# Performance work log

Hardware: AMD Instinct MI355X
Metric: run time of the kernel (lower is better)

## Reference

```python
import jax, jax.numpy as jnp
import numpy as np

B, H, S, D = 2, 16, 2048, 64  # depth = dmodel / num_heads
DMODEL = H * D


def setup_inputs() -> dict:
    key = jax.random.key(0)
    kq, kk, kv, kw = jax.random.split(key, 4)
    Q = jax.random.normal(kq, (B, H, S, D), dtype=jnp.float32)
    K = jax.random.normal(kk, (B, H, S, D), dtype=jnp.float32)
    V = jax.random.normal(kv, (B, H, S, D), dtype=jnp.float32)
    W = jax.random.normal(kw, (DMODEL, DMODEL), dtype=jnp.float32) * (1.0 / np.sqrt(DMODEL))
    b = jnp.zeros((DMODEL,), dtype=jnp.float32)
    return {"Q": Q, "K": K, "V": V, "W": W, "b": b}


def reference(Q, K, V, W, b):
    depth = Q.shape[-1]
    # scores: (B, H, S, S) -- full score matrix, matching the original math
    scores = jnp.einsum('bhqd,bhkd->bhqk', Q, K) / jnp.sqrt(jnp.float32(depth))
    attn = jax.nn.softmax(scores, axis=-1)
    vals = jnp.einsum('bhqk,bhkd->bhqd', attn, V)          # (B, H, S, D)
    vals = jnp.transpose(vals, (0, 2, 1, 3))               # (B, S, H, D)
    concat = vals.reshape(vals.shape[0], vals.shape[1], -1)  # (B, S, dmodel)
    return concat @ W + b
```

## Files before the change

kernel.cpp:

```cpp
#include <hip/hip_runtime.h>
#include <hip/hip_bf16.h>


typedef float  f32x16 __attribute__((ext_vector_type(16)));
typedef float  f32x4v __attribute__((ext_vector_type(4)));
typedef float  f32x2v __attribute__((ext_vector_type(2)));
typedef __bf16 bf16x8 __attribute__((ext_vector_type(8)));
typedef __bf16 bf16x4 __attribute__((ext_vector_type(4)));
typedef __bf16 bf16x2 __attribute__((ext_vector_type(2)));

static constexpr int Bn = 2, Hn = 16, Sn = 2048, Dn = 64, DM = 1024;
static constexpr size_t QKV_ELEMS = (size_t)Bn * Hn * Sn * Dn;

#define QSCALE 0.18033688011112042f

#if __has_builtin(__builtin_amdgcn_cvt_pk_bf16_f32)
static __device__ __forceinline__ unsigned pack2(float a, float b) {
  bf16x2 t = __builtin_amdgcn_cvt_pk_bf16_f32(a, b);
  union { bf16x2 v; unsigned u; } c; c.v = t; return c.u;
}
#else
static __device__ __forceinline__ unsigned pack2(float a, float b) {
  union { __bf16 h; unsigned short s; } ua, ub;
  ua.h = (__bf16)a; ub.h = (__bf16)b;
  return (unsigned)ua.s | ((unsigned)ub.s << 16);
}
#endif

static __device__ __forceinline__ void unzip8(const unsigned* wds, bf16x8* r0, bf16x8* r1) {
  union { unsigned u[4]; bf16x8 v; } a, b;
#pragma unroll
  for (int i = 0; i < 4; ++i) {
    unsigned lo = wds[2 * i], hi = wds[2 * i + 1];
    a.u[i] = (lo & 0xffffu) | (hi << 16);
    b.u[i] = (lo >> 16) | (hi & 0xffff0000u);
  }
  *r0 = a.v; *r1 = b.v;
}

__global__ __launch_bounds__(256) void convert_all(
    const float* __restrict__ q, const float* __restrict__ k,
    const float* __restrict__ v, const float* __restrict__ w,
    __bf16* __restrict__ qo, __bf16* __restrict__ ko,
    __bf16* __restrict__ vt, __bf16* __restrict__ wt) {
  __shared__ __bf16 T[64][74];
  const int bid = blockIdx.x, t = threadIdx.x;

  if (bid < 4096) {
    const int z = bid >> 11;
    const int bx = bid & 2047;
    const float* src = z ? k : q;
    __bf16* dst      = z ? ko : qo;
    const float scale = z ? 1.0f : QSCALE;
    size_t i = ((size_t)bx * 256 + t) * 8;
    f32x4v a = *(const f32x4v*)(src + i);
    f32x4v b = *(const f32x4v*)(src + i + 4);
    bf16x8 o;
#pragma unroll
    for (int j = 0; j < 4; ++j) { o[j] = (__bf16)(a[j] * scale); o[4 + j] = (__bf16)(b[j] * scale); }
    *(bf16x8*)(dst + i) = o;
    return;
  }

  const float* s0;
  __bf16* dst0;
  size_t dst_stride;
  {
    const int r = t >> 2, c0 = (t & 3) * 16;
    if (bid < 5120) {
      const int idx = bid - 4096;
      const int kv0 = (idx & 31) * 64, bh = idx >> 5;
      s0 = v + ((size_t)bh * Sn + kv0 + r) * Dn + c0;
      dst0 = vt + (size_t)bh * Dn * Sn + kv0;
      dst_stride = Sn;
    } else {
      const int idx = bid - 5120;
      const int nt = (idx & 15) * 64, kt = (idx >> 4) * 64;
      s0 = w + (size_t)(kt + r) * DM + nt + c0;
      dst0 = wt + (size_t)nt * DM + kt;
      dst_stride = DM;
    }
    union { bf16x8 v8; unsigned u[4]; } o0, o1;
#pragma unroll
    for (int i = 0; i < 2; ++i) {
      f32x4v f = *(const f32x4v*)(s0 + i * 4);
#pragma unroll
      for (int j = 0; j < 4; ++j) o0.v8[i * 4 + j] = (__bf16)f[j];
    }
#pragma unroll
    for (int i = 0; i < 2; ++i) {
      f32x4v f = *(const f32x4v*)(s0 + 8 + i * 4);
#pragma unroll
      for (int j = 0; j < 4; ++j) o1.v8[i * 4 + j] = (__bf16)f[j];
    }
#pragma unroll
    for (int j = 0; j < 4; ++j) {
      *(unsigned*)&T[r][c0 + 2 * j]     = o0.u[j];
      *(unsigned*)&T[r][c0 + 8 + 2 * j] = o1.u[j];
    }
  }
  __syncthreads();
  const int rp = t >> 3, k0 = (t & 7) * 8;
  unsigned wds[8];
#pragma unroll
  for (int i = 0; i < 8; ++i) wds[i] = *(const unsigned*)&T[k0 + i][2 * rp];
  bf16x8 r0, r1; unzip8(wds, &r0, &r1);
  __bf16* d0 = dst0 + (size_t)(2 * rp) * dst_stride + k0;
  *(bf16x8*)d0 = r0;
  *(bf16x8*)(d0 + dst_stride) = r1;
}

__global__ __launch_bounds__(256, 3) void attn(
    const __bf16* __restrict__ Qb, const __bf16* __restrict__ Kb,
    const __bf16* __restrict__ Vtg, __bf16* __restrict__ Cc) {
  const int tid = threadIdx.x;
  const int wave = tid >> 6, lane = tid & 63;
  const int ln = lane & 31, g = lane >> 5;
  const int qg = wave >> 1, kh = wave & 1;
  const int qb = blockIdx.x, h = blockIdx.y, bz = blockIdx.z;

  __shared__ __bf16 smem[2][2][64][72];
  __bf16 (*Ks)[64][72] = smem[0];
  __bf16 (*Vs)[64][72] = smem[1];

  const size_t hoff = (size_t)(bz * Hn + h) * Sn * Dn;
  const __bf16* Qp = Qb + hoff + (size_t)(qb * 128 + qg * 64) * Dn;
  const __bf16* Kp = Kb + hoff;
  const __bf16* Vp = Vtg + hoff;

  bf16x8 qf[2][4];
#pragma unroll
  for (int qt = 0; qt < 2; ++qt)
#pragma unroll
    for (int ks = 0; ks < 4; ++ks)
      qf[qt][ks] = *(const bf16x8*)(Qp + (size_t)(qt * 32 + ln) * Dn + ks * 16 + g * 8);

  const int sr = tid >> 2, sc = (tid & 3) * 16;
  const __bf16* kbase = Kp + (size_t)sr * Dn + sc;
  const __bf16* vbase = Vp + (size_t)sr * Sn + sc;

  bf16x8 k0r = *(const bf16x8*)kbase, k1r = *(const bf16x8*)(kbase + 8);
  bf16x8 v0r = *(const bf16x8*)vbase, v1r = *(const bf16x8*)(vbase + 8);
  *(bf16x8*)&Ks[0][sr][sc]     = k0r;
  *(bf16x8*)&Ks[0][sr][sc + 8] = k1r;
  *(bf16x8*)&Vs[0][sr][sc]     = v0r;
  *(bf16x8*)&Vs[0][sr][sc + 8] = v1r;
  k0r = *(const bf16x8*)(kbase + (size_t)64 * Dn);
  k1r = *(const bf16x8*)(kbase + (size_t)64 * Dn + 8);
  v0r = *(const bf16x8*)(vbase + 64);
  v1r = *(const bf16x8*)(vbase + 64 + 8);
  __syncthreads();

  f32x16 O[2][2] = {{{}, {}}, {{}, {}}};
  float Lown[2] = {0.0f, 0.0f};
  constexpr int NT = Sn / 64;

  for (int kt = 0; kt < NT; ++kt) {
    const int buf = kt & 1;

    bf16x8 kf[4];
#pragma unroll
    for (int ks = 0; ks < 4; ++ks)
      kf[ks] = *(const bf16x8*)&Ks[buf][kh * 32 + ln][ks * 16 + g * 8];

    unsigned w[2][8];
#pragma unroll
    for (int qt = 0; qt < 2; ++qt) {
      f32x16 s = {};
#pragma unroll
      for (int ks = 0; ks < 4; ++ks)
        s = __builtin_amdgcn_mfma_f32_32x32x16_bf16(kf[ks], qf[qt][ks], s, 0, 0, 0);
      float p[16];
#pragma unroll
      for (int r = 0; r < 16; ++r) p[r] = __builtin_amdgcn_exp2f(s[r]);
      f32x2v s2 = {0.0f, 0.0f};
#pragma unroll
      for (int tt = 0; tt < 8; ++tt) { f32x2v t2 = {p[2 * tt], p[2 * tt + 1]}; s2 += t2; }
      Lown[qt] += s2[0] + s2[1];
#pragma unroll
      for (int tt = 0; tt < 8; ++tt) w[qt][tt] = pack2(p[2 * tt], p[2 * tt + 1]);
    }

    if (kt + 1 < NT) {
      const int nb = buf ^ 1;
      *(bf16x8*)&Ks[nb][sr][sc]     = k0r;
      *(bf16x8*)&Ks[nb][sr][sc + 8] = k1r;
      *(bf16x8*)&Vs[nb][sr][sc]     = v0r;
      *(bf16x8*)&Vs[nb][sr][sc + 8] = v1r;
      if (kt + 2 < NT) {
        const __bf16* kp = kbase + (size_t)(kt + 2) * 64 * Dn;
        k0r = *(const bf16x8*)kp; k1r = *(const bf16x8*)(kp + 8);
        const __bf16* vp = vbase + (kt + 2) * 64;
        v0r = *(const bf16x8*)vp; v1r = *(const bf16x8*)(vp + 8);
      }
    }

#pragma unroll
    for (int s4 = 0; s4 < 2; ++s4) {
      const int cb = kh * 32 + s4 * 16 + g * 4;
      union { bf16x4 h[2]; bf16x8 v; } vf0, vf1;
      vf0.h[0] = *(const bf16x4*)&Vs[buf][ln][cb];
      vf0.h[1] = *(const bf16x4*)&Vs[buf][ln][cb + 8];
      vf1.h[0] = *(const bf16x4*)&Vs[buf][32 + ln][cb];
      vf1.h[1] = *(const bf16x4*)&Vs[buf][32 + ln][cb + 8];
#pragma unroll
      for (int qt = 0; qt < 2; ++qt) {
        union { unsigned u[4]; bf16x8 v; } pu;
        pu.u[0] = w[qt][s4 * 4 + 0];
        pu.u[1] = w[qt][s4 * 4 + 1];
        pu.u[2] = w[qt][s4 * 4 + 2];
        pu.u[3] = w[qt][s4 * 4 + 3];
        O[qt][0] = __builtin_amdgcn_mfma_f32_32x32x16_bf16(vf0.v, pu.v, O[qt][0], 0, 0, 0);
        O[qt][1] = __builtin_amdgcn_mfma_f32_32x32x16_bf16(vf1.v, pu.v, O[qt][1], 0, 0, 0);
      }
    }
    __syncthreads();
  }

  float Lred[2];
#pragma unroll
  for (int qt = 0; qt < 2; ++qt) Lred[qt] = Lown[qt] + __shfl_xor(Lown[qt], 32);

  float* Ex = (float*)smem;
  const int slot = (qg * 64 + lane) * 68;
  if (kh == 1) {
#pragma unroll
    for (int qt = 0; qt < 2; ++qt)
#pragma unroll
      for (int dh = 0; dh < 2; ++dh)
#pragma unroll
        for (int i = 0; i < 4; ++i) {
          f32x4v t = {O[qt][dh][4 * i], O[qt][dh][4 * i + 1],
                      O[qt][dh][4 * i + 2], O[qt][dh][4 * i + 3]};
          *(f32x4v*)&Ex[slot + qt * 32 + dh * 16 + 4 * i] = t;
        }
    Ex[slot + 64] = Lred[0];
    Ex[slot + 65] = Lred[1];
  }
  __syncthreads();
  float inv[2] = {0.0f, 0.0f};
  if (kh == 0) {
#pragma unroll
    for (int qt = 0; qt < 2; ++qt)
#pragma unroll
      for (int dh = 0; dh < 2; ++dh)
#pragma unroll
        for (int i = 0; i < 4; ++i) {
          f32x4v t = *(const f32x4v*)&Ex[slot + qt * 32 + dh * 16 + 4 * i];
#pragma unroll
          for (int c = 0; c < 4; ++c) O[qt][dh][4 * i + c] += t[c];
        }
    inv[0] = 1.0f / (Lred[0] + Ex[slot + 64]);
    inv[1] = 1.0f / (Lred[1] + Ex[slot + 65]);
  }
  __syncthreads();
  __bf16* T = (__bf16*)smem;
  if (kh == 0) {
#pragma unroll
    for (int qt = 0; qt < 2; ++qt)
#pragma unroll
      for (int dh = 0; dh < 2; ++dh)
#pragma unroll
        for (int a = 0; a < 4; ++a) {
          bf16x4 t4;
#pragma unroll
          for (int c = 0; c < 4; ++c) t4[c] = (__bf16)(O[qt][dh][4 * a + c] * inv[qt]);
          *(bf16x4*)&T[(qg * 64 + qt * 32 + ln) * 72 + dh * 32 + 8 * a + 4 * g] = t4;
        }
  }
  __syncthreads();
  const int q0 = qb * 128;
#pragma unroll
  for (int i = 0; i < 4; ++i) {
    const int rq = i * 32 + (tid >> 3);
    const int c8 = (tid & 7) * 8;
    bf16x8 o = *(const bf16x8*)&T[rq * 72 + c8];
    size_t base = (((size_t)bz * Sn + q0 + rq) * Hn + h) * Dn + c8;
    *(bf16x8*)&Cc[base] = o;
  }
}

__global__ __launch_bounds__(256, 2) void proj(
    const __bf16* __restrict__ A, const __bf16* __restrict__ Wt,
    const float* __restrict__ bias, float* __restrict__ out) {
  const int tid = threadIdx.x, wave = tid >> 6, lane = tid & 63;
  const int ln = lane & 31, g = lane >> 5;
  const int bm = blockIdx.x, bn = blockIdx.y;
  __shared__ __bf16 As[2][128][72];
  __shared__ __bf16 Bs[2][64][72];
  const int ar = tid >> 1, ac = (tid & 1) * 32;
  const int br = tid >> 2, bc = (tid & 3) * 16;
  f32x16 acc0 = {}, acc1 = {};
  const __bf16* Ap = A + (size_t)(bm * 128) * DM;
  const __bf16* Wp = Wt + (size_t)(bn * 64) * DM;

  bf16x8 a0, a1, a2, a3, b0, b1;
  {
    const __bf16* ap = Ap + (size_t)ar * DM + ac;
    a0 = *(const bf16x8*)ap;        a1 = *(const bf16x8*)(ap + 8);
    a2 = *(const bf16x8*)(ap + 16); a3 = *(const bf16x8*)(ap + 24);
    const __bf16* wp = Wp + (size_t)br * DM + bc;
    b0 = *(const bf16x8*)wp; b1 = *(const bf16x8*)(wp + 8);
  }
  *(bf16x8*)&As[0][ar][ac]      = a0;
  *(bf16x8*)&As[0][ar][ac + 8]  = a1;
  *(bf16x8*)&As[0][ar][ac + 16] = a2;
  *(bf16x8*)&As[0][ar][ac + 24] = a3;
  *(bf16x8*)&Bs[0][br][bc]      = b0;
  *(bf16x8*)&Bs[0][br][bc + 8]  = b1;
  {
    const __bf16* ap = Ap + (size_t)ar * DM + 64 + ac;
    a0 = *(const bf16x8*)ap;        a1 = *(const bf16x8*)(ap + 8);
    a2 = *(const bf16x8*)(ap + 16); a3 = *(const bf16x8*)(ap + 24);
    const __bf16* wp = Wp + (size_t)br * DM + 64 + bc;
    b0 = *(const bf16x8*)wp; b1 = *(const bf16x8*)(wp + 8);
  }
  __syncthreads();

  constexpr int KT = DM / 64;
  for (int kt = 0; kt < KT; ++kt) {
    const int buf = kt & 1;
#pragma unroll
    for (int ks = 0; ks < 4; ++ks) {
      bf16x8 af  = *(const bf16x8*)&As[buf][wave * 32 + ln][ks * 16 + g * 8];
      bf16x8 wf0 = *(const bf16x8*)&Bs[buf][ln][ks * 16 + g * 8];
      bf16x8 wf1 = *(const bf16x8*)&Bs[buf][32 + ln][ks * 16 + g * 8];
      acc0 = __builtin_amdgcn_mfma_f32_32x32x16_bf16(af, wf0, acc0, 0, 0, 0);
      acc1 = __builtin_amdgcn_mfma_f32_32x32x16_bf16(af, wf1, acc1, 0, 0, 0);
    }
    if (kt + 1 < KT) {
      const int nb = buf ^ 1;
      *(bf16x8*)&As[nb][ar][ac]      = a0;
      *(bf16x8*)&As[nb][ar][ac + 8]  = a1;
      *(bf16x8*)&As[nb][ar][ac + 16] = a2;
      *(bf16x8*)&As[nb][ar][ac + 24] = a3;
      *(bf16x8*)&Bs[nb][br][bc]      = b0;
      *(bf16x8*)&Bs[nb][br][bc + 8]  = b1;
      if (kt + 2 < KT) {
        const __bf16* ap = Ap + (size_t)ar * DM + (kt + 2) * 64 + ac;
        a0 = *(const bf16x8*)ap;        a1 = *(const bf16x8*)(ap + 8);
        a2 = *(const bf16x8*)(ap + 16); a3 = *(const bf16x8*)(ap + 24);
        const __bf16* wp = Wp + (size_t)br * DM + (kt + 2) * 64 + bc;
        b0 = *(const bf16x8*)wp; b1 = *(const bf16x8*)(wp + 8);
      }
    }
    __syncthreads();
  }
  float bv0 = bias[bn * 64 + ln], bv1 = bias[bn * 64 + 32 + ln];
#pragma unroll
  for (int r = 0; r < 16; ++r) {
    int row = bm * 128 + wave * 32 + (r & 3) + ((r >> 2) << 3) + (g << 2);
    out[(size_t)row * DM + bn * 64 + ln]      = acc0[r] + bv0;
    out[(size_t)row * DM + bn * 64 + 32 + ln] = acc1[r] + bv1;
  }
}

extern "C" void kernel_launch(void* const* d_in, const int* in_sizes, int n_in,
                              void* d_out, int out_size, void* d_ws, size_t ws_size,
                              hipStream_t stream) {
  const float* Q = (const float*)d_in[0];
  const float* K = (const float*)d_in[1];
  const float* V = (const float*)d_in[2];
  const float* W = (const float*)d_in[3];
  const float* b = (const float*)d_in[4];
  float* out = (float*)d_out;

  __bf16* ws  = (__bf16*)d_ws;
  __bf16* Qb  = ws;
  __bf16* Kb  = Qb + QKV_ELEMS;
  __bf16* Vtg = Kb + QKV_ELEMS;
  __bf16* Cc  = Vtg + QKV_ELEMS;
  __bf16* Wt  = Cc + QKV_ELEMS;

  convert_all<<<dim3(5376, 1, 1), 256, 0, stream>>>(Q, K, V, W, Qb, Kb, Vtg, Wt);
  attn<<<dim3(Sn / 128, Hn, Bn), 256, 0, stream>>>(Qb, Kb, Vtg, Cc);
  proj<<<dim3(Bn * Sn / 128, DM / 64, 1), 256, 0, stream>>>(Cc, Wt, b, out);
}
```

Measured before the change: 159.2 us.

## Pad V tile stride in attention LDS and use 512-thread projection blocks

The attention kernel changes the V shared-memory tile row stride from 72 to 76 bf16 elements. Because the new stride is not 16-byte aligned, V stores are split into 8-byte pieces. The aim is to cut LDS bank conflicts on the bf16x4 V fragment reads. The projection GEMM moves from 4 to 8 waves per block, with each wave owning one 32x32 output tile instead of two, for more wave-level parallelism and smaller per-thread loads. In exchange, the attention kernel issues more store instructions and uses slightly more LDS, and the projection kernel doubles its threads per block while keeping the same tile size.

```diff
diff --git a/kernel.cpp b/kernel.cpp
--- a/kernel.cpp
+++ b/kernel.cpp
@@ -119,9 +119,9 @@
   const int qg = wave >> 1, kh = wave & 1;
   const int qb = blockIdx.x, h = blockIdx.y, bz = blockIdx.z;
 
-  __shared__ __bf16 smem[2][2][64][72];
-  __bf16 (*Ks)[64][72] = smem[0];
-  __bf16 (*Vs)[64][72] = smem[1];
+  __shared__ char pool[2 * 64 * 72 * 2 + 2 * 64 * 76 * 2];
+  __bf16 (*Ks)[64][72] = (__bf16(*)[64][72])pool;
+  __bf16 (*Vs)[64][76] = (__bf16(*)[64][76])(pool + 2 * 64 * 72 * 2);
 
   const size_t hoff = (size_t)(bz * Hn + h) * Sn * Dn;
   const __bf16* Qp = Qb + hoff + (size_t)(qb * 128 + qg * 64) * Dn;
@@ -141,10 +141,15 @@
 
   bf16x8 k0r = *(const bf16x8*)kbase, k1r = *(const bf16x8*)(kbase + 8);
   bf16x8 v0r = *(const bf16x8*)vbase, v1r = *(const bf16x8*)(vbase + 8);
-  *(bf16x8*)&Ks[0][sr][sc]     = k0r;
-  *(bf16x8*)&Ks[0][sr][sc + 8] = k1r;
-  *(bf16x8*)&Vs[0][sr][sc]     = v0r;
-  *(bf16x8*)&Vs[0][sr][sc + 8] = v1r;
+  {
+    *(bf16x8*)&Ks[0][sr][sc]     = k0r;
+    *(bf16x8*)&Ks[0][sr][sc + 8] = k1r;
+    union { bf16x8 v; bf16x4 h[2]; } u0, u1; u0.v = v0r; u1.v = v1r;
+    *(bf16x4*)&Vs[0][sr][sc]      = u0.h[0];
+    *(bf16x4*)&Vs[0][sr][sc + 4]  = u0.h[1];
+    *(bf16x4*)&Vs[0][sr][sc + 8]  = u1.h[0];
+    *(bf16x4*)&Vs[0][sr][sc + 12] = u1.h[1];
+  }
   k0r = *(const bf16x8*)(kbase + (size_t)64 * Dn);
   k1r = *(const bf16x8*)(kbase + (size_t)64 * Dn + 8);
   v0r = *(const bf16x8*)(vbase + 64);
@@ -185,8 +190,11 @@
       const int nb = buf ^ 1;
       *(bf16x8*)&Ks[nb][sr][sc]     = k0r;
       *(bf16x8*)&Ks[nb][sr][sc + 8] = k1r;
-      *(bf16x8*)&Vs[nb][sr][sc]     = v0r;
-      *(bf16x8*)&Vs[nb][sr][sc + 8] = v1r;
+      union { bf16x8 v; bf16x4 h[2]; } u0, u1; u0.v = v0r; u1.v = v1r;
+      *(bf16x4*)&Vs[nb][sr][sc]      = u0.h[0];
+      *(bf16x4*)&Vs[nb][sr][sc + 4]  = u0.h[1];
+      *(bf16x4*)&Vs[nb][sr][sc + 8]  = u1.h[0];
+      *(bf16x4*)&Vs[nb][sr][sc + 12] = u1.h[1];
       if (kt + 2 < NT) {
         const __bf16* kp = kbase + (size_t)(kt + 2) * 64 * Dn;
         k0r = *(const bf16x8*)kp; k1r = *(const bf16x8*)(kp + 8);
@@ -221,7 +229,7 @@
 #pragma unroll
   for (int qt = 0; qt < 2; ++qt) Lred[qt] = Lown[qt] + __shfl_xor(Lown[qt], 32);
 
-  float* Ex = (float*)smem;
+  float* Ex = (float*)pool;
   const int slot = (qg * 64 + lane) * 68;
   if (kh == 1) {
 #pragma unroll
@@ -254,7 +262,7 @@
     inv[1] = 1.0f / (Lred[1] + Ex[slot + 65]);
   }
   __syncthreads();
-  __bf16* T = (__bf16*)smem;
+  __bf16* T = (__bf16*)pool;
   if (kh == 0) {
 #pragma unroll
     for (int qt = 0; qt < 2; ++qt)
@@ -280,40 +288,34 @@
   }
 }
 
-__global__ __launch_bounds__(256, 2) void proj(
+__global__ __launch_bounds__(512, 2) void proj(
     const __bf16* __restrict__ A, const __bf16* __restrict__ Wt,
     const float* __restrict__ bias, float* __restrict__ out) {
   const int tid = threadIdx.x, wave = tid >> 6, lane = tid & 63;
   const int ln = lane & 31, g = lane >> 5;
+  const int mq = wave >> 1, nh = wave & 1;
   const int bm = blockIdx.x, bn = blockIdx.y;
   __shared__ __bf16 As[2][128][72];
   __shared__ __bf16 Bs[2][64][72];
-  const int ar = tid >> 1, ac = (tid & 1) * 32;
-  const int br = tid >> 2, bc = (tid & 3) * 16;
-  f32x16 acc0 = {}, acc1 = {};
+  const int ar = tid >> 2, ac = (tid & 3) * 16;
+  const int rb = tid >> 3, cb = (tid & 7) * 8;
+  f32x16 acc = {};
   const __bf16* Ap = A + (size_t)(bm * 128) * DM;
   const __bf16* Wp = Wt + (size_t)(bn * 64) * DM;
 
-  bf16x8 a0, a1, a2, a3, b0, b1;
+  bf16x8 a0, a1, b0;
   {
     const __bf16* ap = Ap + (size_t)ar * DM + ac;
-    a0 = *(const bf16x8*)ap;        a1 = *(const bf16x8*)(ap + 8);
-    a2 = *(const bf16x8*)(ap + 16); a3 = *(const bf16x8*)(ap + 24);
-    const __bf16* wp = Wp + (size_t)br * DM + bc;
-    b0 = *(const bf16x8*)wp; b1 = *(const bf16x8*)(wp + 8);
-  }
-  *(bf16x8*)&As[0][ar][ac]      = a0;
-  *(bf16x8*)&As[0][ar][ac + 8]  = a1;
-  *(bf16x8*)&As[0][ar][ac + 16] = a2;
-  *(bf16x8*)&As[0][ar][ac + 24] = a3;
-  *(bf16x8*)&Bs[0][br][bc]      = b0;
-  *(bf16x8*)&Bs[0][br][bc + 8]  = b1;
+    a0 = *(const bf16x8*)ap; a1 = *(const bf16x8*)(ap + 8);
+    b0 = *(const bf16x8*)(Wp + (size_t)rb * DM + cb);
+  }
+  *(bf16x8*)&As[0][ar][ac]     = a0;
+  *(bf16x8*)&As[0][ar][ac + 8] = a1;
+  *(bf16x8*)&Bs[0][rb][cb]     = b0;
   {
     const __bf16* ap = Ap + (size_t)ar * DM + 64 + ac;
-    a0 = *(const bf16x8*)ap;        a1 = *(const bf16x8*)(ap + 8);
-    a2 = *(const bf16x8*)(ap + 16); a3 = *(const bf16x8*)(ap + 24);
-    const __bf16* wp = Wp + (size_t)br * DM + 64 + bc;
-    b0 = *(const bf16x8*)wp; b1 = *(const bf16x8*)(wp + 8);
+    a0 = *(const bf16x8*)ap; a1 = *(const bf16x8*)(ap + 8);
+    b0 = *(const bf16x8*)(Wp + (size_t)rb * DM + 64 + cb);
   }
   __syncthreads();
 
@@ -322,36 +324,28 @@
     const int buf = kt & 1;
 #pragma unroll
     for (int ks = 0; ks < 4; ++ks) {
-      bf16x8 af  = *(const bf16x8*)&As[buf][wave * 32 + ln][ks * 16 + g * 8];
-      bf16x8 wf0 = *(const bf16x8*)&Bs[buf][ln][ks * 16 + g * 8];
-      bf16x8 wf1 = *(const bf16x8*)&Bs[buf][32 + ln][ks * 16 + g * 8];
-      acc0 = __builtin_amdgcn_mfma_f32_32x32x16_bf16(af, wf0, acc0, 0, 0, 0);
-      acc1 = __builtin_amdgcn_mfma_f32_32x32x16_bf16(af, wf1, acc1, 0, 0, 0);
+      bf16x8 af = *(const bf16x8*)&As[buf][mq * 32 + ln][ks * 16 + g * 8];
+      bf16x8 wf = *(const bf16x8*)&Bs[buf][nh * 32 + ln][ks * 16 + g * 8];
+      acc = __builtin_amdgcn_mfma_f32_32x32x16_bf16(af, wf, acc, 0, 0, 0);
     }
     if (kt + 1 < KT) {
       const int nb = buf ^ 1;
-      *(bf16x8*)&As[nb][ar][ac]      = a0;
-      *(bf16x8*)&As[nb][ar][ac + 8]  = a1;
-      *(bf16x8*)&As[nb][ar][ac + 16] = a2;
-      *(bf16x8*)&As[nb][ar][ac + 24] = a3;
-      *(bf16x8*)&Bs[nb][br][bc]      = b0;
-      *(bf16x8*)&Bs[nb][br][bc + 8]  = b1;
+      *(bf16x8*)&As[nb][ar][ac]     = a0;
+      *(bf16x8*)&As[nb][ar][ac + 8] = a1;
+      *(bf16x8*)&Bs[nb][rb][cb]     = b0;
       if (kt + 2 < KT) {
         const __bf16* ap = Ap + (size_t)ar * DM + (kt + 2) * 64 + ac;
-        a0 = *(const bf16x8*)ap;        a1 = *(const bf16x8*)(ap + 8);
-        a2 = *(const bf16x8*)(ap + 16); a3 = *(const bf16x8*)(ap + 24);
-        const __bf16* wp = Wp + (size_t)br * DM + (kt + 2) * 64 + bc;
-        b0 = *(const bf16x8*)wp; b1 = *(const bf16x8*)(wp + 8);
+        a0 = *(const bf16x8*)ap; a1 = *(const bf16x8*)(ap + 8);
+        b0 = *(const bf16x8*)(Wp + (size_t)rb * DM + (kt + 2) * 64 + cb);
       }
     }
     __syncthreads();
   }
-  float bv0 = bias[bn * 64 + ln], bv1 = bias[bn * 64 + 32 + ln];
+  const float bv = bias[bn * 64 + nh * 32 + ln];
 #pragma unroll
   for (int r = 0; r < 16; ++r) {
-    int row = bm * 128 + wave * 32 + (r & 3) + ((r >> 2) << 3) + (g << 2);
-    out[(size_t)row * DM + bn * 64 + ln]      = acc0[r] + bv0;
-    out[(size_t)row * DM + bn * 64 + 32 + ln] = acc1[r] + bv1;
+    int row = bm * 128 + mq * 32 + (r & 3) + 8 * (r >> 2) + 4 * g;
+    out[(size_t)row * DM + bn * 64 + nh * 32 + ln] = acc[r] + bv;
   }
 }
 
@@ -374,5 +368,5 @@
 
   convert_all<<<dim3(5376, 1, 1), 256, 0, stream>>>(Q, K, V, W, Qb, Kb, Vtg, Wt);
   attn<<<dim3(Sn / 128, Hn, Bn), 256, 0, stream>>>(Qb, Kb, Vtg, Cc);
-  proj<<<dim3(Bn * Sn / 128, DM / 64, 1), 256, 0, stream>>>(Cc, Wt, b, out);
-}
+  proj<<<dim3(Bn * Sn / 128, DM / 64, 1), 512, 0, stream>>>(Cc, Wt, b, out);
+}
```

Result: slower. 165.9 us (+4.2%).
